# Optimization experiments

Hardware: AMD Instinct MI355X
Metric: run time of the kernel (lower is better)

Reference implementation:

```python
import jax, jax.numpy as jnp
import numpy as np


def _quantize(x, weight):
    # x: (B, D, H, W); weight: (D, K)
    B, D, H, W = x.shape
    K = weight.shape[1]
    xf = x.reshape(B, D, H * W)  # (B, D, N)
    x2 = jnp.sum(xf * xf, axis=1)                      # (B, N)
    cross = jnp.einsum('bdn,dk->bnk', xf, weight)       # (B, N, K)
    e2 = jnp.sum(weight * weight, axis=0)               # (K,)
    d2 = x2[..., None] - 2.0 * cross + e2               # (B, N, K)
    argmin = jnp.argmin(d2, axis=-1)                    # (B, N)
    # gather codes: (B, N, D) -> (B, D, N) -> (B, D, H, W)
    quant = weight.T[argmin]                            # (B, N, D)
    result = jnp.transpose(quant, (0, 2, 1)).reshape(B, D, H, W)
    return result, argmin.reshape(B, H, W)


def setup_inputs() -> dict:
    key = jax.random.key(0)
    k1, k2 = jax.random.split(key)
    x = jax.random.normal(k1, (32, 256, 32, 32), dtype=jnp.float32)
    weight = jax.random.uniform(k2, (256, 512), dtype=jnp.float32)  # torch.rand init
    return {"x": x, "weight": weight}


def reference(x, weight):
    result, argmin = _quantize(x, weight)
    return result, argmin
```

## Files before the change

### kernel.cpp

```cpp
#include <hip/hip_runtime.h>

typedef __attribute__((ext_vector_type(8))) short bf16x8;
typedef __attribute__((ext_vector_type(16))) float f32x16;

__device__ __forceinline__ bool lex_lt(float av, int ai, float bv, int bi) {
  return av < bv || (av == bv && ai < bi);
}

__device__ __forceinline__ unsigned bf16_rne(float v) {
  unsigned u = __float_as_uint(v);
  return (u + 0x7fffu + ((u >> 16) & 1u)) >> 16;
}

__global__ __launch_bounds__(256) void vq_pre(
    const float* __restrict__ w, float* __restrict__ e2,
    short* __restrict__ wtil, float* __restrict__ wT) {
  int blk = blockIdx.x;
  if (blk < 64) {
    int gid = blk * 256 + threadIdx.x;
    int n  = gid & 511;
    int kg = gid >> 9;
    bf16x8 hv, lv;
    float vv[8];
#pragma unroll
    for (int j = 0; j < 8; ++j) {
      float v = w[(kg * 8 + j) * 512 + n];
      vv[j] = v;
      unsigned h = bf16_rne(v);
      float hf = __uint_as_float(h << 16);
      unsigned l = bf16_rne(v - hf);
      hv[j] = (short)h;
      lv[j] = (short)l;
    }
    short* dst = wtil + (size_t)gid * 8;
    *(bf16x8*)dst = hv;
    *(bf16x8*)(dst + 131072) = lv;
    if (wT) {
      float* p = wT + (size_t)n * 256 + kg * 8;
      *(float4*)p       = make_float4(vv[0], vv[1], vv[2], vv[3]);
      *(float4*)(p + 4) = make_float4(vv[4], vv[5], vv[6], vv[7]);
    }
  } else {
    int t = (blk - 64) * 256 + threadIdx.x;
    int k = t >> 2;
    int part = t & 3;
    double s = 0.0;
#pragma unroll 8
    for (int d = part * 64; d < part * 64 + 64; ++d) {
      double v = (double)w[d * 512 + k];
      s = fma(v, v, s);
    }
    s += __shfl_xor(s, 1);
    s += __shfl_xor(s, 2);
    if (part == 0) e2[k] = (float)s;
  }
}

__global__ __launch_bounds__(512, 4) void vq_main(
    const float* __restrict__ x, const float* __restrict__ w,
    const float* __restrict__ e2g, const short* __restrict__ wtil,
    const float* __restrict__ wT,
    float* __restrict__ out, float* __restrict__ arg_out) {
  __shared__ __align__(16) char arena[76032];
  short* xh  = (short*)arena;
  short* xl  = (short*)(arena + 32768);
  float* e2s = (float*)(arena + 65536);
  float* tv1 = (float*)(arena + 67584);
  float* tv2 = (float*)(arena + 69632);
  int*   ti1 = (int*)(arena + 71680);
  int*   ti2 = (int*)(arena + 73728);
  int*   pickS = (int*)(arena + 75776);

  const int tid = threadIdx.x;
  const int b  = blockIdx.x >> 4;
  const int n0 = (blockIdx.x & 15) << 6;
  const float* xbase = x + (size_t)b * 262144 + n0;

  {
    const int n4  = tid & 15;
    const int kg  = tid >> 4;
    float4 v[8];
#pragma unroll
    for (int j = 0; j < 8; ++j)
      v[j] = *(const float4*)(xbase + (size_t)(kg * 8 + j) * 1024 + (n4 << 2));
#pragma unroll
    for (int i = 0; i < 4; ++i) {
      int m = (n4 << 2) + i;
      bf16x8 hv, lv;
#pragma unroll
      for (int j = 0; j < 8; ++j) {
        float f = (i == 0) ? v[j].x : (i == 1) ? v[j].y : (i == 2) ? v[j].z : v[j].w;
        unsigned h = bf16_rne(f);
        unsigned l = bf16_rne(f - __uint_as_float(h << 16));
        hv[j] = (short)h;
        lv[j] = (short)l;
      }
      int off = (m << 8) + ((kg ^ (m & 7)) << 3);
      *(bf16x8*)&xh[off] = hv;
      *(bf16x8*)&xl[off] = lv;
    }
    e2s[tid & 511] = e2g[tid & 511];
  }
  __syncthreads();

  const int lane = tid & 63;
  const int wv   = tid >> 6;
  const int ln   = lane & 31;
  const int half = lane >> 5;
  const int wb   = wv << 6;

  f32x16 acc[2][2];
#pragma unroll
  for (int ct = 0; ct < 2; ++ct)
#pragma unroll
    for (int pt = 0; pt < 2; ++pt)
#pragma unroll
      for (int r = 0; r < 16; ++r) acc[ct][pt][r] = 0.f;

  const int m0 = ln, m1 = 32 + ln;
  const int a0base = m0 << 8, a1base = m1 << 8;
  const int a0sw = m0 & 7, a1sw = m1 & 7;

  size_t bofs[2];
#pragma unroll
  for (int ct = 0; ct < 2; ++ct) bofs[ct] = (size_t)((wb + (ct << 5) + ln) << 3);

  bf16x8 pch[2], pcl[2];
#pragma unroll
  for (int ct = 0; ct < 2; ++ct) {
    const short* p = wtil + ((size_t)half << 12) + bofs[ct];
    pch[ct] = *(const bf16x8*)p;
    pcl[ct] = *(const bf16x8*)(p + 131072);
  }

#pragma unroll
  for (int ch = 0; ch < 16; ++ch) {
    const int kg = (ch << 1) + half;
    bf16x8 xh0 = *(const bf16x8*)&xh[a0base + ((kg ^ a0sw) << 3)];
    bf16x8 xl0 = *(const bf16x8*)&xl[a0base + ((kg ^ a0sw) << 3)];
    bf16x8 xh1 = *(const bf16x8*)&xh[a1base + ((kg ^ a1sw) << 3)];
    bf16x8 xl1 = *(const bf16x8*)&xl[a1base + ((kg ^ a1sw) << 3)];
    bf16x8 cfh[2], cfl[2];
#pragma unroll
    for (int ct = 0; ct < 2; ++ct) { cfh[ct] = pch[ct]; cfl[ct] = pcl[ct]; }
    if (ch < 15) {
      const int kgn = ((ch + 1) << 1) + half;
#pragma unroll
      for (int ct = 0; ct < 2; ++ct) {
        const short* p = wtil + ((size_t)kgn << 12) + bofs[ct];
        pch[ct] = *(const bf16x8*)p;
        pcl[ct] = *(const bf16x8*)(p + 131072);
      }
    }
#pragma unroll
    for (int ct = 0; ct < 2; ++ct) {
      acc[ct][0] = __builtin_amdgcn_mfma_f32_32x32x16_bf16(cfh[ct], xh0, acc[ct][0], 0, 0, 0);
      acc[ct][0] = __builtin_amdgcn_mfma_f32_32x32x16_bf16(cfh[ct], xl0, acc[ct][0], 0, 0, 0);
      acc[ct][0] = __builtin_amdgcn_mfma_f32_32x32x16_bf16(cfl[ct], xh0, acc[ct][0], 0, 0, 0);
      acc[ct][1] = __builtin_amdgcn_mfma_f32_32x32x16_bf16(cfh[ct], xh1, acc[ct][1], 0, 0, 0);
      acc[ct][1] = __builtin_amdgcn_mfma_f32_32x32x16_bf16(cfh[ct], xl1, acc[ct][1], 0, 0, 0);
      acc[ct][1] = __builtin_amdgcn_mfma_f32_32x32x16_bf16(cfl[ct], xh1, acc[ct][1], 0, 0, 0);
    }
  }

  float e2r[2][16];
#pragma unroll
  for (int ct = 0; ct < 2; ++ct)
#pragma unroll
    for (int r = 0; r < 16; ++r)
      e2r[ct][r] = e2s[wb + (ct << 5) + (r & 3) + ((r >> 2) << 3) + (half << 2)];

#pragma unroll
  for (int pt = 0; pt < 2; ++pt) {
    float v1 = 3.4e38f, v2 = 3.4e38f;
    int i1 = 0x7fffffff, i2 = 0x7fffffff;
#pragma unroll
    for (int ct = 0; ct < 2; ++ct) {
#pragma unroll
      for (int r = 0; r < 16; ++r) {
        int k = wb + (ct << 5) + (r & 3) + ((r >> 2) << 3) + (half << 2);
        float s = fmaf(-2.f, acc[ct][pt][r], e2r[ct][r]);
        if (lex_lt(s, k, v1, i1)) { v2 = v1; i2 = i1; v1 = s; i1 = k; }
        else if (lex_lt(s, k, v2, i2)) { v2 = s; i2 = k; }
      }
    }
    {
      float ov1 = __shfl_xor(v1, 32);
      int   oi1 = __shfl_xor(i1, 32);
      float ov2 = __shfl_xor(v2, 32);
      int   oi2 = __shfl_xor(i2, 32);
      bool aFirst = lex_lt(v1, i1, ov1, oi1);
      float nv1 = aFirst ? v1 : ov1;  int ni1 = aFirst ? i1 : oi1;
      float cv  = aFirst ? ov1 : v1;  int ci  = aFirst ? oi1 : i1;
      float sv  = aFirst ? v2 : ov2;  int si  = aFirst ? i2 : oi2;
      bool cFirst = lex_lt(cv, ci, sv, si);
      v1 = nv1; i1 = ni1;
      v2 = cFirst ? cv : sv; i2 = cFirst ? ci : si;
    }
    if (half == 0) {
      int s = (wv << 6) + (pt << 5) + ln;
      tv1[s] = v1; ti1[s] = i1; tv2[s] = v2; ti2[s] = i2;
    }
  }
  __syncthreads();

  if (tid < 64) {
    int row = tid;
    float v1 = 3.4e38f, v2 = 3.4e38f;
    int i1 = 0x7fffffff, i2 = 0x7fffffff;
#pragma unroll
    for (int wvv = 0; wvv < 8; ++wvv) {
      int s = (wvv << 6) + row;
      float a1 = tv1[s]; int ai = ti1[s];
      float a2 = tv2[s]; int bi = ti2[s];
      if (lex_lt(a1, ai, v1, i1)) { v2 = v1; i2 = i1; v1 = a1; i1 = ai; }
      else if (lex_lt(a1, ai, v2, i2)) { v2 = a1; i2 = ai; }
      if (lex_lt(a2, bi, v1, i1)) { v2 = v1; i2 = i1; v1 = a2; i1 = bi; }
      else if (lex_lt(a2, bi, v2, i2)) { v2 = a2; i2 = bi; }
    }
    int pick = i1;
    if (v2 - v1 < 0.01f) {
      double s1 = 0.0, s2 = 0.0;
      const float* xp = x + (size_t)b * 262144 + n0 + row;
#pragma unroll 4
      for (int k = 0; k < 256; ++k) {
        double xv = (double)xp[(size_t)k * 1024];
        double w1 = (double)w[k * 512 + i1];
        double w2 = (double)w[k * 512 + i2];
        double t1 = xv - w1, t2 = xv - w2;
        s1 = fma(t1, t1, s1);
        s2 = fma(t2, t2, s2);
      }
      if (s2 < s1 || (s2 == s1 && i2 < i1)) pick = i2;
    }
    int p = b * 1024 + n0 + row;
    arg_out[p] = (float)pick;
    pickS[row] = pick;
  }
  __syncthreads();

  if (wT) {
    float* gbuf = (float*)arena;
    {
      const int pos  = tid >> 3;
      const int dseg = tid & 7;
      const float* wrow = wT + (size_t)pickS[pos] * 256;
#pragma unroll
      for (int j = 0; j < 8; ++j) {
        float4 v = *(const float4*)(wrow + j * 32 + dseg * 4);
        int base = pos * 265 + j * 33 + dseg * 4;
        gbuf[base]     = v.x;
        gbuf[base + 1] = v.y;
        gbuf[base + 2] = v.z;
        gbuf[base + 3] = v.w;
      }
    }
    __syncthreads();
    {
      const int nn0 = (tid & 15) << 2;
      const int d0g = tid >> 4;
      float* obase = out + (size_t)b * 262144 + n0 + nn0;
#pragma unroll
      for (int dg = 0; dg < 8; ++dg) {
        int d = d0g + (dg << 5);
        int sa = (d >> 5) * 33 + (d & 31);
        float4 o;
        o.x = gbuf[(nn0 + 0) * 265 + sa];
        o.y = gbuf[(nn0 + 1) * 265 + sa];
        o.z = gbuf[(nn0 + 2) * 265 + sa];
        o.w = gbuf[(nn0 + 3) * 265 + sa];
        *(float4*)(obase + (size_t)d * 1024) = o;
      }
    }
  } else {
    const int nn0 = (tid & 15) << 2;
    const int d0g = tid >> 4;
    int pk0 = pickS[nn0], pk1 = pickS[nn0 + 1], pk2 = pickS[nn0 + 2], pk3 = pickS[nn0 + 3];
    float* obase = out + (size_t)b * 262144 + n0 + nn0;
#pragma unroll
    for (int dg = 0; dg < 8; ++dg) {
      int d = d0g + (dg << 5);
      const float* wr = w + d * 512;
      float4 o = make_float4(wr[pk0], wr[pk1], wr[pk2], wr[pk3]);
      *(float4*)(obase + (size_t)d * 1024) = o;
    }
  }
}

extern "C" void kernel_launch(void* const* d_in, const int* in_sizes, int n_in,
                              void* d_out, int out_size, void* d_ws, size_t ws_size,
                              hipStream_t stream) {
  const float* x = (const float*)d_in[0];
  const float* w = (const float*)d_in[1];
  float* out  = (float*)d_out;
  float* argf = out + 8388608;
  float* e2   = (float*)d_ws;
  short* wtil = (short*)((char*)d_ws + 2048);
  size_t need = 2048 + 524288 + 524288;
  float* wT   = (ws_size >= need) ? (float*)((char*)d_ws + 2048 + 524288) : nullptr;

  vq_pre<<<72, 256, 0, stream>>>(w, e2, wtil, wT);
  vq_main<<<512, 512, 0, stream>>>(x, w, e2, wtil, wT, out, argf);
}
```

Baseline: 137.1 us.

## Double per-block position tile and parallelize fp64 tie refinement across waves

Each block now handles 128 positions instead of 64. That doubles reuse of each codebook fragment loaded from global memory across four MFMA accumulator tiles, and halves the grid to 256 blocks with roughly 148KB of LDS per block. The fp64 near-tie recheck moves from a serial loop in one wave to a per-row reduction across 64 lanes spread over all waves. The bf16 hi/lo split is also packed two values at a time. The cost is lower occupancy (two blocks per SM bound, likely one given the LDS size) and fewer blocks than CUs on a large GPU, which may leave compute units idle.

```diff
diff --git a/kernel.cpp b/kernel.cpp
--- a/kernel.cpp
+++ b/kernel.cpp
@@ -10,6 +10,10 @@
 __device__ __forceinline__ unsigned bf16_rne(float v) {
   unsigned u = __float_as_uint(v);
   return (u + 0x7fffu + ((u >> 16) & 1u)) >> 16;
+}
+
+__device__ __forceinline__ unsigned pk_bf16(float a, float b) {
+  return bf16_rne(a) | (bf16_rne(b) << 16);
 }
 
 __global__ __launch_bounds__(256) void vq_pre(
@@ -56,50 +60,61 @@
   }
 }
 
-__global__ __launch_bounds__(512, 4) void vq_main(
+__global__ __launch_bounds__(512, 2) void vq_main(
     const float* __restrict__ x, const float* __restrict__ w,
     const float* __restrict__ e2g, const short* __restrict__ wtil,
     const float* __restrict__ wT,
     float* __restrict__ out, float* __restrict__ arg_out) {
-  __shared__ __align__(16) char arena[76032];
-  short* xh  = (short*)arena;
-  short* xl  = (short*)(arena + 32768);
-  float* e2s = (float*)(arena + 65536);
-  float* tv1 = (float*)(arena + 67584);
-  float* tv2 = (float*)(arena + 69632);
-  int*   ti1 = (int*)(arena + 71680);
-  int*   ti2 = (int*)(arena + 73728);
-  int*   pickS = (int*)(arena + 75776);
+  __shared__ __align__(16) char arena[151552];
+  short* xh   = (short*)arena;
+  short* xl   = (short*)(arena + 65536);
+  float* e2s  = (float*)(arena + 131072);
+  float* tv1  = (float*)(arena + 133120);
+  float* tv2  = (float*)(arena + 137216);
+  int*   ti1  = (int*)(arena + 141312);
+  int*   ti2  = (int*)(arena + 145408);
+  int*   p1S  = (int*)(arena + 149504);
+  int*   p2S  = (int*)(arena + 150016);
+  int*   needS= (int*)(arena + 150528);
+  int*   rpickS=(int*)(arena + 151040);
+  float* gbuf = (float*)arena;
 
   const int tid = threadIdx.x;
-  const int b  = blockIdx.x >> 4;
-  const int n0 = (blockIdx.x & 15) << 6;
+  const int b  = blockIdx.x >> 3;
+  const int n0 = (blockIdx.x & 7) << 7;
   const float* xbase = x + (size_t)b * 262144 + n0;
 
   {
-    const int n4  = tid & 15;
-    const int kg  = tid >> 4;
-    float4 v[8];
-#pragma unroll
-    for (int j = 0; j < 8; ++j)
-      v[j] = *(const float4*)(xbase + (size_t)(kg * 8 + j) * 1024 + (n4 << 2));
-#pragma unroll
-    for (int i = 0; i < 4; ++i) {
-      int m = (n4 << 2) + i;
-      bf16x8 hv, lv;
-#pragma unroll
-      for (int j = 0; j < 8; ++j) {
-        float f = (i == 0) ? v[j].x : (i == 1) ? v[j].y : (i == 2) ? v[j].z : v[j].w;
-        unsigned h = bf16_rne(f);
-        unsigned l = bf16_rne(f - __uint_as_float(h << 16));
-        hv[j] = (short)h;
-        lv[j] = (short)l;
-      }
-      int off = (m << 8) + ((kg ^ (m & 7)) << 3);
-      *(bf16x8*)&xh[off] = hv;
-      *(bf16x8*)&xl[off] = lv;
-    }
-    e2s[tid & 511] = e2g[tid & 511];
+    const int n4  = tid & 31;
+    const int kgp = tid >> 5;
+#pragma unroll
+    for (int rep = 0; rep < 2; ++rep) {
+      int kg = kgp + (rep << 4);
+      float4 v[8];
+#pragma unroll
+      for (int j = 0; j < 8; ++j)
+        v[j] = *(const float4*)(xbase + (size_t)(kg * 8 + j) * 1024 + (n4 << 2));
+#pragma unroll
+      for (int i = 0; i < 4; ++i) {
+        int m = (n4 << 2) + i;
+        union { int w4[4]; bf16x8 v8; } H, L;
+#pragma unroll
+        for (int jj = 0; jj < 4; ++jj) {
+          float a = (i == 0) ? v[2*jj].x : (i == 1) ? v[2*jj].y : (i == 2) ? v[2*jj].z : v[2*jj].w;
+          float c = (i == 0) ? v[2*jj+1].x : (i == 1) ? v[2*jj+1].y : (i == 2) ? v[2*jj+1].z : v[2*jj+1].w;
+          unsigned hu = pk_bf16(a, c);
+          float haf = __uint_as_float(hu << 16);
+          float hcf = __uint_as_float(hu & 0xffff0000u);
+          unsigned lu = pk_bf16(a - haf, c - hcf);
+          H.w4[jj] = (int)hu;
+          L.w4[jj] = (int)lu;
+        }
+        int off = (m << 8) + ((kg ^ (m & 7)) << 3);
+        *(bf16x8*)&xh[off] = H.v8;
+        *(bf16x8*)&xl[off] = L.v8;
+      }
+    }
+    e2s[tid] = e2g[tid];
   }
   __syncthreads();
 
@@ -109,26 +124,25 @@
   const int half = lane >> 5;
   const int wb   = wv << 6;
 
-  f32x16 acc[2][2];
+  f32x16 acc[2][4];
 #pragma unroll
   for (int ct = 0; ct < 2; ++ct)
 #pragma unroll
-    for (int pt = 0; pt < 2; ++pt)
+    for (int pt = 0; pt < 4; ++pt)
 #pragma unroll
       for (int r = 0; r < 16; ++r) acc[ct][pt][r] = 0.f;
 
-  const int m0 = ln, m1 = 32 + ln;
-  const int a0base = m0 << 8, a1base = m1 << 8;
-  const int a0sw = m0 & 7, a1sw = m1 & 7;
-
-  size_t bofs[2];
-#pragma unroll
-  for (int ct = 0; ct < 2; ++ct) bofs[ct] = (size_t)((wb + (ct << 5) + ln) << 3);
+  const int asw = ln & 7;
+  const int abase = ln << 8;
+
+  int bofs[2];
+#pragma unroll
+  for (int ct = 0; ct < 2; ++ct) bofs[ct] = (wb + (ct << 5) + ln) << 3;
 
   bf16x8 pch[2], pcl[2];
 #pragma unroll
   for (int ct = 0; ct < 2; ++ct) {
-    const short* p = wtil + ((size_t)half << 12) + bofs[ct];
+    const short* p = wtil + (half << 12) + bofs[ct];
     pch[ct] = *(const bf16x8*)p;
     pcl[ct] = *(const bf16x8*)(p + 131072);
   }
@@ -136,10 +150,13 @@
 #pragma unroll
   for (int ch = 0; ch < 16; ++ch) {
     const int kg = (ch << 1) + half;
-    bf16x8 xh0 = *(const bf16x8*)&xh[a0base + ((kg ^ a0sw) << 3)];
-    bf16x8 xl0 = *(const bf16x8*)&xl[a0base + ((kg ^ a0sw) << 3)];
-    bf16x8 xh1 = *(const bf16x8*)&xh[a1base + ((kg ^ a1sw) << 3)];
-    bf16x8 xl1 = *(const bf16x8*)&xl[a1base + ((kg ^ a1sw) << 3)];
+    const int ao = abase + ((kg ^ asw) << 3);
+    bf16x8 xf[4], xg[4];
+#pragma unroll
+    for (int pt = 0; pt < 4; ++pt) {
+      xf[pt] = *(const bf16x8*)&xh[ao + (pt << 13)];
+      xg[pt] = *(const bf16x8*)&xl[ao + (pt << 13)];
+    }
     bf16x8 cfh[2], cfl[2];
 #pragma unroll
     for (int ct = 0; ct < 2; ++ct) { cfh[ct] = pch[ct]; cfl[ct] = pcl[ct]; }
@@ -147,20 +164,19 @@
       const int kgn = ((ch + 1) << 1) + half;
 #pragma unroll
       for (int ct = 0; ct < 2; ++ct) {
-        const short* p = wtil + ((size_t)kgn << 12) + bofs[ct];
+        const short* p = wtil + (kgn << 12) + bofs[ct];
         pch[ct] = *(const bf16x8*)p;
         pcl[ct] = *(const bf16x8*)(p + 131072);
       }
     }
 #pragma unroll
-    for (int ct = 0; ct < 2; ++ct) {
-      acc[ct][0] = __builtin_amdgcn_mfma_f32_32x32x16_bf16(cfh[ct], xh0, acc[ct][0], 0, 0, 0);
-      acc[ct][0] = __builtin_amdgcn_mfma_f32_32x32x16_bf16(cfh[ct], xl0, acc[ct][0], 0, 0, 0);
-      acc[ct][0] = __builtin_amdgcn_mfma_f32_32x32x16_bf16(cfl[ct], xh0, acc[ct][0], 0, 0, 0);
-      acc[ct][1] = __builtin_amdgcn_mfma_f32_32x32x16_bf16(cfh[ct], xh1, acc[ct][1], 0, 0, 0);
-      acc[ct][1] = __builtin_amdgcn_mfma_f32_32x32x16_bf16(cfh[ct], xl1, acc[ct][1], 0, 0, 0);
-      acc[ct][1] = __builtin_amdgcn_mfma_f32_32x32x16_bf16(cfl[ct], xh1, acc[ct][1], 0, 0, 0);
-    }
+    for (int ct = 0; ct < 2; ++ct)
+#pragma unroll
+      for (int pt = 0; pt < 4; ++pt) {
+        acc[ct][pt] = __builtin_amdgcn_mfma_f32_32x32x16_bf16(cfh[ct], xf[pt], acc[ct][pt], 0, 0, 0);
+        acc[ct][pt] = __builtin_amdgcn_mfma_f32_32x32x16_bf16(cfh[ct], xg[pt], acc[ct][pt], 0, 0, 0);
+        acc[ct][pt] = __builtin_amdgcn_mfma_f32_32x32x16_bf16(cfl[ct], xf[pt], acc[ct][pt], 0, 0, 0);
+      }
   }
 
   float e2r[2][16];
@@ -171,7 +187,7 @@
       e2r[ct][r] = e2s[wb + (ct << 5) + (r & 3) + ((r >> 2) << 3) + (half << 2)];
 
 #pragma unroll
-  for (int pt = 0; pt < 2; ++pt) {
+  for (int pt = 0; pt < 4; ++pt) {
     float v1 = 3.4e38f, v2 = 3.4e38f;
     int i1 = 0x7fffffff, i2 = 0x7fffffff;
 #pragma unroll
@@ -198,19 +214,19 @@
       v2 = cFirst ? cv : sv; i2 = cFirst ? ci : si;
     }
     if (half == 0) {
-      int s = (wv << 6) + (pt << 5) + ln;
+      int s = (wv << 7) + (pt << 5) + ln;
       tv1[s] = v1; ti1[s] = i1; tv2[s] = v2; ti2[s] = i2;
     }
   }
   __syncthreads();
 
-  if (tid < 64) {
+  if (tid < 128) {
     int row = tid;
     float v1 = 3.4e38f, v2 = 3.4e38f;
     int i1 = 0x7fffffff, i2 = 0x7fffffff;
 #pragma unroll
     for (int wvv = 0; wvv < 8; ++wvv) {
-      int s = (wvv << 6) + row;
+      int s = (wvv << 7) + row;
       float a1 = tv1[s]; int ai = ti1[s];
       float a2 = tv2[s]; int bi = ti2[s];
       if (lex_lt(a1, ai, v1, i1)) { v2 = v1; i2 = i1; v1 = a1; i1 = ai; }
@@ -218,12 +234,22 @@
       if (lex_lt(a2, bi, v1, i1)) { v2 = v1; i2 = i1; v1 = a2; i1 = bi; }
       else if (lex_lt(a2, bi, v2, i2)) { v2 = a2; i2 = bi; }
     }
-    int pick = i1;
-    if (v2 - v1 < 0.01f) {
+    p1S[row] = i1; p2S[row] = i2;
+    needS[row] = (v2 - v1 < 0.01f) ? 1 : 0;
+    rpickS[row] = i1;
+  }
+  __syncthreads();
+
+  for (int t = 0; t < 16; ++t) {
+    int row = (t << 3) + wv;
+    if (needS[row]) {
+      int i1 = p1S[row], i2 = p2S[row];
+      const float* xp = x + (size_t)b * 262144 + n0 + row;
       double s1 = 0.0, s2 = 0.0;
-      const float* xp = x + (size_t)b * 262144 + n0 + row;
-#pragma unroll 4
-      for (int k = 0; k < 256; ++k) {
+      int k0 = lane << 2;
+#pragma unroll
+      for (int i = 0; i < 4; ++i) {
+        int k = k0 + i;
         double xv = (double)xp[(size_t)k * 1024];
         double w1 = (double)w[k * 512 + i1];
         double w2 = (double)w[k * 512 + i2];
@@ -231,24 +257,28 @@
         s1 = fma(t1, t1, s1);
         s2 = fma(t2, t2, s2);
       }
-      if (s2 < s1 || (s2 == s1 && i2 < i1)) pick = i2;
-    }
-    int p = b * 1024 + n0 + row;
-    arg_out[p] = (float)pick;
-    pickS[row] = pick;
+#pragma unroll
+      for (int off = 32; off >= 1; off >>= 1) {
+        s1 += __shfl_xor(s1, off);
+        s2 += __shfl_xor(s2, off);
+      }
+      if (lane == 0 && (s2 < s1 || (s2 == s1 && i2 < i1))) rpickS[row] = i2;
+    }
   }
   __syncthreads();
 
+  if (tid < 128) arg_out[b * 1024 + n0 + tid] = (float)rpickS[tid];
+
   if (wT) {
-    float* gbuf = (float*)arena;
     {
-      const int pos  = tid >> 3;
-      const int dseg = tid & 7;
-      const float* wrow = wT + (size_t)pickS[pos] * 256;
-#pragma unroll
-      for (int j = 0; j < 8; ++j) {
-        float4 v = *(const float4*)(wrow + j * 32 + dseg * 4);
-        int base = pos * 265 + j * 33 + dseg * 4;
+      const int pos  = tid >> 2;
+      const int dseg = tid & 3;
+      const float* wrow = wT + (size_t)rpickS[pos] * 256;
+#pragma unroll
+      for (int j = 0; j < 16; ++j) {
+        int d = (j << 4) + (dseg << 2);
+        float4 v = *(const float4*)(wrow + d);
+        int base = pos * 265 + d + (d >> 5);
         gbuf[base]     = v.x;
         gbuf[base + 1] = v.y;
         gbuf[base + 2] = v.z;
@@ -257,13 +287,13 @@
     }
     __syncthreads();
     {
-      const int nn0 = (tid & 15) << 2;
-      const int d0g = tid >> 4;
+      const int nn0 = (tid & 31) << 2;
+      const int d0g = tid >> 5;
       float* obase = out + (size_t)b * 262144 + n0 + nn0;
 #pragma unroll
-      for (int dg = 0; dg < 8; ++dg) {
-        int d = d0g + (dg << 5);
-        int sa = (d >> 5) * 33 + (d & 31);
+      for (int dg = 0; dg < 16; ++dg) {
+        int d = d0g + (dg << 4);
+        int sa = d + (d >> 5);
         float4 o;
         o.x = gbuf[(nn0 + 0) * 265 + sa];
         o.y = gbuf[(nn0 + 1) * 265 + sa];
@@ -273,13 +303,13 @@
       }
     }
   } else {
-    const int nn0 = (tid & 15) << 2;
-    const int d0g = tid >> 4;
-    int pk0 = pickS[nn0], pk1 = pickS[nn0 + 1], pk2 = pickS[nn0 + 2], pk3 = pickS[nn0 + 3];
+    const int nn0 = (tid & 31) << 2;
+    const int d0g = tid >> 5;
+    int pk0 = rpickS[nn0], pk1 = rpickS[nn0 + 1], pk2 = rpickS[nn0 + 2], pk3 = rpickS[nn0 + 3];
     float* obase = out + (size_t)b * 262144 + n0 + nn0;
 #pragma unroll
-    for (int dg = 0; dg < 8; ++dg) {
-      int d = d0g + (dg << 5);
+    for (int dg = 0; dg < 16; ++dg) {
+      int d = d0g + (dg << 4);
       const float* wr = w + d * 512;
       float4 o = make_float4(wr[pk0], wr[pk1], wr[pk2], wr[pk3]);
       *(float4*)(obase + (size_t)d * 1024) = o;
@@ -300,5 +330,5 @@
   float* wT   = (ws_size >= need) ? (float*)((char*)d_ws + 2048 + 524288) : nullptr;
 
   vq_pre<<<72, 256, 0, stream>>>(w, e2, wtil, wT);
-  vq_main<<<512, 512, 0, stream>>>(x, w, e2, wtil, wT, out, argf);
-}
+  vq_main<<<256, 512, 0, stream>>>(x, w, e2, wtil, wT, out, argf);
+}
```

Result: faster. 124.1 us (-9.5%).
